# Optimization experiments

Measured on AMD Instinct MI355X. Metric: run time of the kernel, lower is better.

The kernel has to match this reference:

```python
import jax, jax.numpy as jnp
import numpy as np

NV, NSEG, SEGSZ, GRID = 778, 16, 49, 32
SCALE_FACTOR = 0.1


def grid_sample_3d(vol, pts):
    """Trilinear grid_sample, align_corners=True, zeros padding.
    vol: [D,H,W]; pts: [N,3] with (x,y,z) in [-1,1] (x indexes W, z indexes D).
    """
    D, H, W = vol.shape
    fx = (pts[:, 0] + 1.0) * 0.5 * (W - 1)
    fy = (pts[:, 1] + 1.0) * 0.5 * (H - 1)
    fz = (pts[:, 2] + 1.0) * 0.5 * (D - 1)
    x0f, y0f, z0f = jnp.floor(fx), jnp.floor(fy), jnp.floor(fz)
    wx, wy, wz = fx - x0f, fy - y0f, fz - z0f
    x0 = x0f.astype(jnp.int32)
    y0 = y0f.astype(jnp.int32)
    z0 = z0f.astype(jnp.int32)
    out = jnp.zeros(pts.shape[0], vol.dtype)
    for dz in (0, 1):
        zz = z0 + dz
        ww_z = wz if dz else (1.0 - wz)
        for dy in (0, 1):
            yy = y0 + dy
            ww_zy = ww_z * (wy if dy else (1.0 - wy))
            for dx in (0, 1):
                xx = x0 + dx
                w = ww_zy * (wx if dx else (1.0 - wx))
                valid = (xx >= 0) & (xx < W) & (yy >= 0) & (yy < H) & (zz >= 0) & (zz < D)
                v = vol[jnp.clip(zz, 0, D - 1), jnp.clip(yy, 0, H - 1), jnp.clip(xx, 0, W - 1)]
                out = out + jnp.where(valid, v, 0.0) * w
    return out


def _boxes(segv):
    # segv: [B,16,S,3] -> center [B,16,3], scale [B,16]  (no_grad in original)
    mn = segv.min(axis=2)
    mx = segv.max(axis=2)
    center = 0.5 * (mn + mx)                       # mean of (min, max)
    scale = (1.0 + SCALE_FACTOR) * 0.5 * (mx - mn).max(axis=-1)
    return jax.lax.stop_gradient(center), jax.lax.stop_gradient(scale)


def _cross_sample(seg_src, center, scale, phi, seg):
    # seg_src [B,I,S,3]; center [B,J,3]; scale [B,J]; phi [J,B,G,G,G]
    B = seg_src.shape[0]
    coords = (seg_src[:, :, None, :, :] - center[:, None, :, None, :]) / scale[:, None, :, None, None]
    pts = coords.transpose(2, 0, 1, 3, 4).reshape(NSEG, B, NSEG * SEGSZ, 3)  # [J,B,M,3]
    vals = jax.vmap(jax.vmap(grid_sample_3d))(phi, pts)                      # [J,B,M]
    vals = vals.reshape(NSEG, B, NSEG, SEGSZ).transpose(1, 2, 0, 3)          # [B,I,J,S]
    phisum = vals.sum(axis=2)                                                # [B,I,S]
    orisum = (vals * scale[:, None, :, None]).sum(axis=2)                    # [B,I,S]
    flat = seg.reshape(-1)
    out = jnp.zeros((B, NV), jnp.float32).at[:, flat].add(phisum.reshape(B, -1))
    ori = jnp.zeros((B, NV), jnp.float32).at[:, flat].add(orisum.reshape(B, -1))
    return out, ori


def setup_inputs() -> dict:
    key = jax.random.key(0)
    k1, k2, k3, k4 = jax.random.split(key, 4)
    bs = 128
    vertices = jax.random.normal(k1, (bs, 2, NV, 3), dtype=jnp.float32)
    seg = jax.random.randint(k2, (NSEG, SEGSZ), 0, NV).astype(jnp.int32)
    phi_right = jax.random.uniform(k3, (NSEG, bs, GRID, GRID, GRID), dtype=jnp.float32)
    phi_left = jax.random.uniform(k4, (NSEG, bs, GRID, GRID, GRID), dtype=jnp.float32)
    return {"vertices": vertices, "phi_right": phi_right, "phi_left": phi_left, "seg": seg}


def reference(vertices, phi_right, phi_left, seg):
    left_vert = vertices[:, 1]   # [B,778,3]
    right_vert = vertices[:, 0]
    segL = left_vert[:, seg]     # [B,16,S,3]
    segR = right_vert[:, seg]
    cL, sL = _boxes(segL)
    cR, sR = _boxes(segR)
    out_left, _ = _cross_sample(segL, cR, sR, phi_right, seg)
    out_right, _ = _cross_sample(segR, cL, sL, phi_left, seg)
    num_hand = 2
    loss = (out_left / num_hand ** 2 + out_right / num_hand ** 2).sum(axis=1)  # [B]
    return loss
```

## Files before the change

### kernel.cpp

```cpp
#include <hip/hip_runtime.h>

#define NVV   778
#define NSEG  16
#define SEGSZ 49
#define GRIDN 32
#define BATCH 128
#define NPTS  (NSEG * SEGSZ)
#define VOLSZ (GRIDN * GRIDN * GRIDN)
#define NVOL  (2 * BATCH * NSEG)
#define NBLK  256
#define VPB   (NVOL / NBLK)

#define H0_FLOATS (16 * 1024)
#define H1_FLOATS (17 * 1024)
#define H0_CHUNKS (H0_FLOATS / 256)
#define H1_CHUNKS (H1_FLOATS / 256)

typedef __attribute__((address_space(1))) const void* as1_t;
typedef __attribute__((address_space(3))) void* as3_t;

#define STREAM(DST, SRC, NCH) \
    for (int c = wv; c < (NCH); c += 16) { \
        __builtin_amdgcn_global_load_lds( \
            (as1_t)((SRC) + c * 256 + lane * 4), \
            (as3_t)((DST) + c * 256), 16, 0, 0); \
    }

#define PV_LOAD(IT, nx, ny, nz) \
    if ((IT) < VPB && tid < NPTS) { \
        int vid_ = bx + NBLK * (IT); \
        int b_   = (vid_ >> 4) & (BATCH - 1); \
        int src_ = (vid_ >> 11) == 0 ? 1 : 0; \
        const float* v_ = vertices + (((size_t)b_ * 2 + src_) * NVV + pvi) * 3; \
        nx = v_[0]; ny = v_[1]; nz = v_[2]; \
    }

__device__ __forceinline__ float taps_half(
    const float* base, int zrel0, bool z0ok, bool z1ok,
    int x0, int y0, float wx, float wy, float wz)
{
    float s = 0.f;
    #pragma unroll
    for (int dz = 0; dz < 2; ++dz) {
        if (!(dz ? z1ok : z0ok)) continue;
        float wwz = dz ? wz : 1.f - wz;
        const float* slab = base + (zrel0 + dz) * (GRIDN * GRIDN);
        #pragma unroll
        for (int dy = 0; dy < 2; ++dy) {
            int yy = y0 + dy;
            if (yy < 0 || yy >= GRIDN) continue;
            float wzy = wwz * (dy ? wy : 1.f - wy);
            const float* row = slab + yy * GRIDN;
            #pragma unroll
            for (int dx = 0; dx < 2; ++dx) {
                int xx = x0 + dx;
                if (xx < 0 || xx >= GRIDN) continue;
                s += wzy * (dx ? wx : 1.f - wx) * row[xx];
            }
        }
    }
    return s;
}

__global__ __launch_bounds__(1024, 4) void sample_kernel(
    const float* __restrict__ vertices, const int* __restrict__ seg,
    const float* __restrict__ phiR, const float* __restrict__ phiL,
    float* __restrict__ loss)
{
    __shared__ __align__(16) float R0[H0_FLOATS];
    __shared__ __align__(16) float R1[H1_FLOATS];
    __shared__ float4 sbox[VPB];
    __shared__ float wsum[16];

    const int tid  = threadIdx.x;
    const int bx   = blockIdx.x;
    const int k    = bx & (NSEG - 1);
    const int wv   = tid >> 6;
    const int lane = tid & 63;

    auto phiPtr = [&](int it) {
        int vid  = bx + NBLK * it;
        int b    = (vid >> 4) & (BATCH - 1);
        int pass = vid >> 11;
        return (pass == 0 ? phiR : phiL) + ((size_t)k * BATCH + b) * VOLSZ;
    };

    {
        const float* p0 = phiPtr(0);
        STREAM(R0, p0, H0_CHUNKS)
    }

    int pvi = (tid < NPTS) ? seg[tid] : 0;

    {
        int vid  = bx + NBLK * wv;
        int bb   = (vid >> 4) & (BATCH - 1);
        int pass = vid >> 11;
        int boxSide = (pass == 0) ? 0 : 1;
        const float* vbox = vertices + ((size_t)bb * 2 + boxSide) * NVV * 3;
        bool act = lane < SEGSZ;
        int vi = act ? seg[k * SEGSZ + lane] : 0;
        const float* v = vbox + (size_t)vi * 3;
        float x = v[0], y = v[1], z = v[2];
        float mnx = act ? x : 1e30f, mxx = act ? x : -1e30f;
        float mny = act ? y : 1e30f, mxy = act ? y : -1e30f;
        float mnz = act ? z : 1e30f, mxz = act ? z : -1e30f;
        #pragma unroll
        for (int m = 32; m; m >>= 1) {
            mnx = fminf(mnx, __shfl_xor(mnx, m));
            mxx = fmaxf(mxx, __shfl_xor(mxx, m));
            mny = fminf(mny, __shfl_xor(mny, m));
            mxy = fmaxf(mxy, __shfl_xor(mxy, m));
            mnz = fminf(mnz, __shfl_xor(mnz, m));
            mxz = fmaxf(mxz, __shfl_xor(mxz, m));
        }
        if (lane == 0) {
            float ext = fmaxf(fmaxf(mxx - mnx, mxy - mny), mxz - mnz);
            sbox[wv] = make_float4(0.5f * (mnx + mxx), 0.5f * (mny + mxy),
                                   0.5f * (mnz + mxz), 1.0f / (0.55f * ext));
        }
    }

    float pvx = 0.f, pvy = 0.f, pvz = 0.f;
    float nvx = 0.f, nvy = 0.f, nvz = 0.f;
    PV_LOAD(0, pvx, pvy, pvz)

    __syncthreads();

    for (int v = 0; v < VPB; ++v) {
        const float* pv_phi = phiPtr(v);

        STREAM(R1, pv_phi + 15 * 1024, H1_CHUNKS)

        float fx = 0.f, fy = 0.f, fz = -2.f;
        if (tid < NPTS) {
            float4 b4 = sbox[v];
            fx = ((pvx - b4.x) * b4.w + 1.f) * 15.5f;
            fy = ((pvy - b4.y) * b4.w + 1.f) * 15.5f;
            fz = ((pvz - b4.z) * b4.w + 1.f) * 15.5f;
        }
        PV_LOAD(v + 1, nvx, nvy, nvz)

        bool inxy = (fx > -1.f && fx < 32.f && fy > -1.f && fy < 32.f);
        float x0f = floorf(fx), y0f = floorf(fy), z0f = floorf(fz);
        float wx = fx - x0f, wy = fy - y0f, wz = fz - z0f;
        int x0 = (int)x0f, y0 = (int)y0f, z0 = (int)z0f;

        float acc = 0.f;
        if (inxy && fz > -1.f && fz < 15.f)
            acc += taps_half(R0, z0, z0 >= 0, true, x0, y0, wx, wy, wz);

        __syncthreads();

        if (v + 1 < VPB) {
            const float* pn_phi = phiPtr(v + 1);
            STREAM(R0, pn_phi, H0_CHUNKS)
        }
        if (inxy && fz >= 15.f && fz < 32.f)
            acc += taps_half(R1, z0 - 15, true, z0 + 1 < GRIDN, x0, y0, wx, wy, wz);

        #pragma unroll
        for (int off = 32; off; off >>= 1)
            acc += __shfl_down(acc, off);
        if (lane == 0) wsum[wv] = acc;
        __syncthreads();
        if (tid == 0) {
            float tot = 0.f;
            #pragma unroll
            for (int i = 0; i < 16; ++i) tot += wsum[i];
            int vid = bx + NBLK * v;
            atomicAdd(loss + ((vid >> 4) & (BATCH - 1)), tot * 0.25f);
        }
        pvx = nvx; pvy = nvy; pvz = nvz;
    }
}

extern "C" void kernel_launch(void* const* d_in, const int* in_sizes, int n_in,
                              void* d_out, int out_size, void* d_ws, size_t ws_size,
                              hipStream_t stream) {
    const float* vertices = (const float*)d_in[0];
    const float* phiR     = (const float*)d_in[1];
    const float* phiL     = (const float*)d_in[2];
    const int*   seg      = (const int*)d_in[3];
    float* loss = (float*)d_out;

    hipMemsetAsync(d_out, 0, (size_t)out_size * sizeof(float), stream);

    sample_kernel<<<NBLK, 1024, 0, stream>>>(vertices, seg, phiR, phiL, loss);
}
```

Measured before the change: 106.4 us.

## Split volume staging into three overlapping z-slabs with explicit vmcnt waits

Replaces the two-half LDS staging of each 32^3 volume with three 12K-float slabs covering overlapping z-ranges, streamed in rotation so that loading the next volume's slabs overlaps sampling from the current ones. __syncthreads is replaced with inline s_waitcnt vmcnt(N) plus s_barrier, so each wait covers only the required slab instead of draining every outstanding load. The point and box vertex loads are also moved ahead of the first stream. The hand-counted vmcnt values are fragile: if the per-thread load count differs from what is assumed, the kernel could read slabs that have not arrived yet.

Result: no change. 107.5 us (+1.1%).

```diff
diff --git a/kernel.cpp b/kernel.cpp
--- a/kernel.cpp
+++ b/kernel.cpp
@@ -11,20 +11,25 @@
 #define NBLK  256
 #define VPB   (NVOL / NBLK)
 
-#define H0_FLOATS (16 * 1024)
-#define H1_FLOATS (17 * 1024)
-#define H0_CHUNKS (H0_FLOATS / 256)
-#define H1_CHUNKS (H1_FLOATS / 256)
+#define PF      (12 * 1024)
 
 typedef __attribute__((address_space(1))) const void* as1_t;
 typedef __attribute__((address_space(3))) void* as3_t;
 
-#define STREAM(DST, SRC, NCH) \
-    for (int c = wv; c < (NCH); c += 16) { \
+#define STREAM(DST, SRC) \
+    { _Pragma("unroll") \
+      for (int c_ = 0; c_ < 3; ++c_) { \
+        int ch_ = c_ * 16 + wv; \
         __builtin_amdgcn_global_load_lds( \
-            (as1_t)((SRC) + c * 256 + lane * 4), \
-            (as3_t)((DST) + c * 256), 16, 0, 0); \
-    }
+            (as1_t)((SRC) + ch_ * 256 + lane * 4), \
+            (as3_t)((DST) + ch_ * 256), 16, 0, 0); \
+      } }
+
+#define FENCE asm volatile("" ::: "memory")
+
+#define WAITB(N) \
+    { asm volatile("s_waitcnt vmcnt(" #N ") lgkmcnt(0)" ::: "memory"); \
+      __builtin_amdgcn_s_barrier(); }
 
 #define PV_LOAD(IT, nx, ny, nz) \
     if ((IT) < VPB && tid < NPTS) { \
@@ -35,7 +40,7 @@
         nx = v_[0]; ny = v_[1]; nz = v_[2]; \
     }
 
-__device__ __forceinline__ float taps_half(
+__device__ __forceinline__ float taps_piece(
     const float* base, int zrel0, bool z0ok, bool z1ok,
     int x0, int y0, float wx, float wy, float wz)
 {
@@ -67,8 +72,9 @@
     const float* __restrict__ phiR, const float* __restrict__ phiL,
     float* __restrict__ loss)
 {
-    __shared__ __align__(16) float R0[H0_FLOATS];
-    __shared__ __align__(16) float R1[H1_FLOATS];
+    __shared__ __align__(16) float B0[PF];
+    __shared__ __align__(16) float B1[PF];
+    __shared__ __align__(16) float B2[PF];
     __shared__ float4 sbox[VPB];
     __shared__ float wsum[16];
 
@@ -85,26 +91,32 @@
         return (pass == 0 ? phiR : phiL) + ((size_t)k * BATCH + b) * VOLSZ;
     };
 
+    int pvi = (tid < NPTS) ? seg[tid] : 0;
+
+    int vidw  = bx + NBLK * wv;
+    int bbw   = (vidw >> 4) & (BATCH - 1);
+    int boxSide = ((vidw >> 11) == 0) ? 0 : 1;
+    bool bact = lane < SEGSZ;
+    int bvi = bact ? seg[k * SEGSZ + lane] : 0;
+    const float* bv = vertices + (((size_t)bbw * 2 + boxSide) * NVV + bvi) * 3;
+    float bxx = bv[0], bxy = bv[1], bxz = bv[2];
+
+    float pvx = 0.f, pvy = 0.f, pvz = 0.f;
+    float nvx = 0.f, nvy = 0.f, nvz = 0.f;
+    PV_LOAD(0, pvx, pvy, pvz)
+
+    FENCE;
     {
         const float* p0 = phiPtr(0);
-        STREAM(R0, p0, H0_CHUNKS)
-    }
-
-    int pvi = (tid < NPTS) ? seg[tid] : 0;
+        STREAM(B0, p0)
+        STREAM(B1, p0 + 11 * 1024)
+    }
+    FENCE;
 
     {
-        int vid  = bx + NBLK * wv;
-        int bb   = (vid >> 4) & (BATCH - 1);
-        int pass = vid >> 11;
-        int boxSide = (pass == 0) ? 0 : 1;
-        const float* vbox = vertices + ((size_t)bb * 2 + boxSide) * NVV * 3;
-        bool act = lane < SEGSZ;
-        int vi = act ? seg[k * SEGSZ + lane] : 0;
-        const float* v = vbox + (size_t)vi * 3;
-        float x = v[0], y = v[1], z = v[2];
-        float mnx = act ? x : 1e30f, mxx = act ? x : -1e30f;
-        float mny = act ? y : 1e30f, mxy = act ? y : -1e30f;
-        float mnz = act ? z : 1e30f, mxz = act ? z : -1e30f;
+        float mnx = bact ? bxx : 1e30f, mxx = bact ? bxx : -1e30f;
+        float mny = bact ? bxy : 1e30f, mxy = bact ? bxy : -1e30f;
+        float mnz = bact ? bxz : 1e30f, mxz = bact ? bxz : -1e30f;
         #pragma unroll
         for (int m = 32; m; m >>= 1) {
             mnx = fminf(mnx, __shfl_xor(mnx, m));
@@ -121,16 +133,11 @@
         }
     }
 
-    float pvx = 0.f, pvy = 0.f, pvz = 0.f;
-    float nvx = 0.f, nvy = 0.f, nvz = 0.f;
-    PV_LOAD(0, pvx, pvy, pvz)
-
-    __syncthreads();
+    WAITB(3)
 
     for (int v = 0; v < VPB; ++v) {
-        const float* pv_phi = phiPtr(v);
-
-        STREAM(R1, pv_phi + 15 * 1024, H1_CHUNKS)
+        const float* pc_phi = phiPtr(v);
+        const bool more = (v + 1 < VPB);
 
         float fx = 0.f, fy = 0.f, fz = -2.f;
         if (tid < NPTS) {
@@ -139,31 +146,46 @@
             fy = ((pvy - b4.y) * b4.w + 1.f) * 15.5f;
             fz = ((pvz - b4.z) * b4.w + 1.f) * 15.5f;
         }
-        PV_LOAD(v + 1, nvx, nvy, nvz)
-
-        bool inxy = (fx > -1.f && fx < 32.f && fy > -1.f && fy < 32.f);
+        bool active = (fx > -1.f && fx < 32.f && fy > -1.f && fy < 32.f &&
+                       fz > -1.f && fz < 32.f);
         float x0f = floorf(fx), y0f = floorf(fy), z0f = floorf(fz);
         float wx = fx - x0f, wy = fy - y0f, wz = fz - z0f;
         int x0 = (int)x0f, y0 = (int)y0f, z0 = (int)z0f;
-
+        int pc = (z0 <= 10) ? 0 : ((z0 <= 21) ? 1 : 2);
         float acc = 0.f;
-        if (inxy && fz > -1.f && fz < 15.f)
-            acc += taps_half(R0, z0, z0 >= 0, true, x0, y0, wx, wy, wz);
-
-        __syncthreads();
-
-        if (v + 1 < VPB) {
-            const float* pn_phi = phiPtr(v + 1);
-            STREAM(R0, pn_phi, H0_CHUNKS)
-        }
-        if (inxy && fz >= 15.f && fz < 32.f)
-            acc += taps_half(R1, z0 - 15, true, z0 + 1 < GRIDN, x0, y0, wx, wy, wz);
+
+        PV_LOAD(v + 1, nvx, nvy, nvz)
+        FENCE;
+        STREAM(B2, pc_phi + 20 * 1024)
+        FENCE;
+        if (active && pc == 0)
+            acc += taps_piece(B0, z0, z0 >= 0, true, x0, y0, wx, wy, wz);
+        WAITB(3)
+
+        if (more) {
+            const float* pn = phiPtr(v + 1);
+            FENCE;
+            STREAM(B0, pn)
+            FENCE;
+        }
+        if (active && pc == 1)
+            acc += taps_piece(B1, z0 - 11, true, true, x0, y0, wx, wy, wz);
+        if (more) { WAITB(3) } else { WAITB(0) }
+
+        if (more) {
+            const float* pn = phiPtr(v + 1);
+            FENCE;
+            STREAM(B1, pn + 11 * 1024)
+            FENCE;
+        }
+        if (active && pc == 2)
+            acc += taps_piece(B2, z0 - 20, true, z0 < 31, x0, y0, wx, wy, wz);
 
         #pragma unroll
         for (int off = 32; off; off >>= 1)
             acc += __shfl_down(acc, off);
         if (lane == 0) wsum[wv] = acc;
-        __syncthreads();
+        if (more) { WAITB(3) } else { WAITB(0) }
         if (tid == 0) {
             float tot = 0.f;
             #pragma unroll
```

## Split each volume's z-halves across two blocks, drop in-block double buffering

Applied to the files above, without the earlier changes.

Doubles the grid to 512 blocks, with each block handling only one z-half of every volume (17 slabs or 16 slabs) in a single LDS buffer. The previous overlapped two-region streaming pipeline and next-vertex prefetch are removed in favour of load, sync, compute per volume. The aim is to halve LDS per block and raise occupancy so other resident blocks hide load latency. In exchange, box computation and vertex loads are duplicated across the two halves, atomics double, and the in-block load/compute overlap is lost.

Measured after the change: 123.1 us. +15.7%, slower.

```diff
diff --git a/kernel.cpp b/kernel.cpp
--- a/kernel.cpp
+++ b/kernel.cpp
@@ -7,100 +7,49 @@
 #define BATCH 128
 #define NPTS  (NSEG * SEGSZ)
 #define VOLSZ (GRIDN * GRIDN * GRIDN)
-#define NVOL  (2 * BATCH * NSEG)
-#define NBLK  256
-#define VPB   (NVOL / NBLK)
+#define NBLK  512
+#define VPB   16
 
-#define H0_FLOATS (16 * 1024)
-#define H1_FLOATS (17 * 1024)
-#define H0_CHUNKS (H0_FLOATS / 256)
-#define H1_CHUNKS (H1_FLOATS / 256)
+#define HALF_MAX_FLOATS (17 * 1024)
 
 typedef __attribute__((address_space(1))) const void* as1_t;
 typedef __attribute__((address_space(3))) void* as3_t;
 
-#define STREAM(DST, SRC, NCH) \
-    for (int c = wv; c < (NCH); c += 16) { \
-        __builtin_amdgcn_global_load_lds( \
-            (as1_t)((SRC) + c * 256 + lane * 4), \
-            (as3_t)((DST) + c * 256), 16, 0, 0); \
-    }
-
-#define PV_LOAD(IT, nx, ny, nz) \
-    if ((IT) < VPB && tid < NPTS) { \
-        int vid_ = bx + NBLK * (IT); \
-        int b_   = (vid_ >> 4) & (BATCH - 1); \
-        int src_ = (vid_ >> 11) == 0 ? 1 : 0; \
-        const float* v_ = vertices + (((size_t)b_ * 2 + src_) * NVV + pvi) * 3; \
-        nx = v_[0]; ny = v_[1]; nz = v_[2]; \
-    }
-
-__device__ __forceinline__ float taps_half(
-    const float* base, int zrel0, bool z0ok, bool z1ok,
-    int x0, int y0, float wx, float wy, float wz)
-{
-    float s = 0.f;
-    #pragma unroll
-    for (int dz = 0; dz < 2; ++dz) {
-        if (!(dz ? z1ok : z0ok)) continue;
-        float wwz = dz ? wz : 1.f - wz;
-        const float* slab = base + (zrel0 + dz) * (GRIDN * GRIDN);
-        #pragma unroll
-        for (int dy = 0; dy < 2; ++dy) {
-            int yy = y0 + dy;
-            if (yy < 0 || yy >= GRIDN) continue;
-            float wzy = wwz * (dy ? wy : 1.f - wy);
-            const float* row = slab + yy * GRIDN;
-            #pragma unroll
-            for (int dx = 0; dx < 2; ++dx) {
-                int xx = x0 + dx;
-                if (xx < 0 || xx >= GRIDN) continue;
-                s += wzy * (dx ? wx : 1.f - wx) * row[xx];
-            }
-        }
-    }
-    return s;
-}
-
-__global__ __launch_bounds__(1024, 4) void sample_kernel(
+__global__ __launch_bounds__(1024, 8) void sample_kernel(
     const float* __restrict__ vertices, const int* __restrict__ seg,
     const float* __restrict__ phiR, const float* __restrict__ phiL,
     float* __restrict__ loss)
 {
-    __shared__ __align__(16) float R0[H0_FLOATS];
-    __shared__ __align__(16) float R1[H1_FLOATS];
+    __shared__ __align__(16) float piece[HALF_MAX_FLOATS];
     __shared__ float4 sbox[VPB];
     __shared__ float wsum[16];
 
     const int tid  = threadIdx.x;
     const int bx   = blockIdx.x;
-    const int k    = bx & (NSEG - 1);
+    const int half = bx >> 8;
+    const int base = bx & 255;
+    const int k    = base & (NSEG - 1);
     const int wv   = tid >> 6;
     const int lane = tid & 63;
 
+    const int   nch  = half ? 64 : 68;
+    const int   soff = half ? 16 * 1024 : 0;
+
     auto phiPtr = [&](int it) {
-        int vid  = bx + NBLK * it;
+        int vid  = base + 256 * it;
         int b    = (vid >> 4) & (BATCH - 1);
         int pass = vid >> 11;
         return (pass == 0 ? phiR : phiL) + ((size_t)k * BATCH + b) * VOLSZ;
     };
 
+    int pvi = (tid < NPTS) ? seg[tid] : 0;
     {
-        const float* p0 = phiPtr(0);
-        STREAM(R0, p0, H0_CHUNKS)
-    }
-
-    int pvi = (tid < NPTS) ? seg[tid] : 0;
-
-    {
-        int vid  = bx + NBLK * wv;
+        int vid  = base + 256 * wv;
         int bb   = (vid >> 4) & (BATCH - 1);
-        int pass = vid >> 11;
-        int boxSide = (pass == 0) ? 0 : 1;
-        const float* vbox = vertices + ((size_t)bb * 2 + boxSide) * NVV * 3;
+        int boxSide = ((vid >> 11) == 0) ? 0 : 1;
         bool act = lane < SEGSZ;
         int vi = act ? seg[k * SEGSZ + lane] : 0;
-        const float* v = vbox + (size_t)vi * 3;
+        const float* v = vertices + (((size_t)bb * 2 + boxSide) * NVV + vi) * 3;
         float x = v[0], y = v[1], z = v[2];
         float mnx = act ? x : 1e30f, mxx = act ? x : -1e30f;
         float mny = act ? y : 1e30f, mxy = act ? y : -1e30f;
@@ -121,43 +70,62 @@
         }
     }
 
-    float pvx = 0.f, pvy = 0.f, pvz = 0.f;
-    float nvx = 0.f, nvy = 0.f, nvz = 0.f;
-    PV_LOAD(0, pvx, pvy, pvz)
+    for (int it = 0; it < VPB; ++it) {
+        const float* src = phiPtr(it) + soff;
 
-    __syncthreads();
+        for (int c = wv; c < nch; c += 16)
+            __builtin_amdgcn_global_load_lds(
+                (as1_t)(src + c * 256 + lane * 4),
+                (as3_t)(piece + c * 256), 16, 0, 0);
 
-    for (int v = 0; v < VPB; ++v) {
-        const float* pv_phi = phiPtr(v);
-
-        STREAM(R1, pv_phi + 15 * 1024, H1_CHUNKS)
-
-        float fx = 0.f, fy = 0.f, fz = -2.f;
+        float pvx = 0.f, pvy = 0.f, pvz = 0.f;
         if (tid < NPTS) {
-            float4 b4 = sbox[v];
-            fx = ((pvx - b4.x) * b4.w + 1.f) * 15.5f;
-            fy = ((pvy - b4.y) * b4.w + 1.f) * 15.5f;
-            fz = ((pvz - b4.z) * b4.w + 1.f) * 15.5f;
+            int vid  = base + 256 * it;
+            int b    = (vid >> 4) & (BATCH - 1);
+            int srcS = (vid >> 11) == 0 ? 1 : 0;
+            const float* v = vertices + (((size_t)b * 2 + srcS) * NVV + pvi) * 3;
+            pvx = v[0]; pvy = v[1]; pvz = v[2];
         }
-        PV_LOAD(v + 1, nvx, nvy, nvz)
-
-        bool inxy = (fx > -1.f && fx < 32.f && fy > -1.f && fy < 32.f);
-        float x0f = floorf(fx), y0f = floorf(fy), z0f = floorf(fz);
-        float wx = fx - x0f, wy = fy - y0f, wz = fz - z0f;
-        int x0 = (int)x0f, y0 = (int)y0f, z0 = (int)z0f;
-
-        float acc = 0.f;
-        if (inxy && fz > -1.f && fz < 15.f)
-            acc += taps_half(R0, z0, z0 >= 0, true, x0, y0, wx, wy, wz);
 
         __syncthreads();
 
-        if (v + 1 < VPB) {
-            const float* pn_phi = phiPtr(v + 1);
-            STREAM(R0, pn_phi, H0_CHUNKS)
+        float acc = 0.f;
+        if (tid < NPTS) {
+            float4 b4 = sbox[it];
+            float fx = ((pvx - b4.x) * b4.w + 1.f) * 15.5f;
+            float fy = ((pvy - b4.y) * b4.w + 1.f) * 15.5f;
+            float fz = ((pvz - b4.z) * b4.w + 1.f) * 15.5f;
+            bool inxy = (fx > -1.f && fx < 32.f && fy > -1.f && fy < 32.f);
+            bool inz  = half ? (fz >= 16.f && fz < 32.f)
+                             : (fz > -1.f && fz < 16.f);
+            if (inxy && inz) {
+                float x0f = floorf(fx), y0f = floorf(fy), z0f = floorf(fz);
+                float wx = fx - x0f, wy = fy - y0f, wz = fz - z0f;
+                int x0 = (int)x0f, y0 = (int)y0f, z0 = (int)z0f;
+                int zr = z0 - (half ? 16 : 0);
+                bool z0ok = half ? true : (z0 >= 0);
+                bool z1ok = half ? (z0 < 31) : true;
+                #pragma unroll
+                for (int dz = 0; dz < 2; ++dz) {
+                    if (!(dz ? z1ok : z0ok)) continue;
+                    float wwz = dz ? wz : 1.f - wz;
+                    const float* slab = piece + (zr + dz) * (GRIDN * GRIDN);
+                    #pragma unroll
+                    for (int dy = 0; dy < 2; ++dy) {
+                        int yy = y0 + dy;
+                        if (yy < 0 || yy >= GRIDN) continue;
+                        float wzy = wwz * (dy ? wy : 1.f - wy);
+                        const float* row = slab + yy * GRIDN;
+                        #pragma unroll
+                        for (int dx = 0; dx < 2; ++dx) {
+                            int xx = x0 + dx;
+                            if (xx < 0 || xx >= GRIDN) continue;
+                            acc += wzy * (dx ? wx : 1.f - wx) * row[xx];
+                        }
+                    }
+                }
+            }
         }
-        if (inxy && fz >= 15.f && fz < 32.f)
-            acc += taps_half(R1, z0 - 15, true, z0 + 1 < GRIDN, x0, y0, wx, wy, wz);
 
         #pragma unroll
         for (int off = 32; off; off >>= 1)
@@ -168,10 +136,9 @@
             float tot = 0.f;
             #pragma unroll
             for (int i = 0; i < 16; ++i) tot += wsum[i];
-            int vid = bx + NBLK * v;
+            int vid = base + 256 * it;
             atomicAdd(loss + ((vid >> 4) & (BATCH - 1)), tot * 0.25f);
         }
-        pvx = nvx; pvy = nvy; pvz = nvz;
     }
 }
 
```

## Split volume into equal 16-slab halves, per-wave atomics, restructure loads

Applied to the files above, without the earlier changes.

The volume is now split into two equal 16-slab halves instead of 16 and 17 slabs with an overlap slab. The straddling z=15/16 case is handled by sampling one tap plane from each buffer, so the LDS streaming loops become fixed four-iteration unrolled loops. The block-level reduction through shared memory and thread 0 is replaced by a per-wave atomicAdd to global memory. The prefetch of the next vertices is moved after the barrier. This trims redundant LDS traffic and one reduction step, at the cost of sixteen times more global atomics per volume.

Measured after the change: 323.3 us. +203.9%, slower.

```diff
diff --git a/kernel.cpp b/kernel.cpp
--- a/kernel.cpp
+++ b/kernel.cpp
@@ -7,56 +7,38 @@
 #define BATCH 128
 #define NPTS  (NSEG * SEGSZ)
 #define VOLSZ (GRIDN * GRIDN * GRIDN)
-#define NVOL  (2 * BATCH * NSEG)
 #define NBLK  256
-#define VPB   (NVOL / NBLK)
+#define VPB   16
 
-#define H0_FLOATS (16 * 1024)
-#define H1_FLOATS (17 * 1024)
-#define H0_CHUNKS (H0_FLOATS / 256)
-#define H1_CHUNKS (H1_FLOATS / 256)
+#define HF (16 * 1024)
 
 typedef __attribute__((address_space(1))) const void* as1_t;
 typedef __attribute__((address_space(3))) void* as3_t;
 
-#define STREAM(DST, SRC, NCH) \
-    for (int c = wv; c < (NCH); c += 16) { \
+#define STREAM(DST, SRC) \
+    { _Pragma("unroll") \
+      for (int c_ = 0; c_ < 4; ++c_) { \
+        int ch_ = c_ * 16 + wv; \
         __builtin_amdgcn_global_load_lds( \
-            (as1_t)((SRC) + c * 256 + lane * 4), \
-            (as3_t)((DST) + c * 256), 16, 0, 0); \
-    }
+            (as1_t)((SRC) + ch_ * 256 + lane * 4), \
+            (as3_t)((DST) + ch_ * 256), 16, 0, 0); \
+      } }
 
-#define PV_LOAD(IT, nx, ny, nz) \
-    if ((IT) < VPB && tid < NPTS) { \
-        int vid_ = bx + NBLK * (IT); \
-        int b_   = (vid_ >> 4) & (BATCH - 1); \
-        int src_ = (vid_ >> 11) == 0 ? 1 : 0; \
-        const float* v_ = vertices + (((size_t)b_ * 2 + src_) * NVV + pvi) * 3; \
-        nx = v_[0]; ny = v_[1]; nz = v_[2]; \
-    }
-
-__device__ __forceinline__ float taps_half(
-    const float* base, int zrel0, bool z0ok, bool z1ok,
-    int x0, int y0, float wx, float wy, float wz)
+__device__ __forceinline__ float tapxy(const float* slab, int x0, int y0,
+                                       float wx, float wy)
 {
     float s = 0.f;
     #pragma unroll
-    for (int dz = 0; dz < 2; ++dz) {
-        if (!(dz ? z1ok : z0ok)) continue;
-        float wwz = dz ? wz : 1.f - wz;
-        const float* slab = base + (zrel0 + dz) * (GRIDN * GRIDN);
+    for (int dy = 0; dy < 2; ++dy) {
+        int yy = y0 + dy;
+        if (yy < 0 || yy >= GRIDN) continue;
+        float wyv = dy ? wy : 1.f - wy;
+        const float* row = slab + yy * GRIDN;
         #pragma unroll
-        for (int dy = 0; dy < 2; ++dy) {
-            int yy = y0 + dy;
-            if (yy < 0 || yy >= GRIDN) continue;
-            float wzy = wwz * (dy ? wy : 1.f - wy);
-            const float* row = slab + yy * GRIDN;
-            #pragma unroll
-            for (int dx = 0; dx < 2; ++dx) {
-                int xx = x0 + dx;
-                if (xx < 0 || xx >= GRIDN) continue;
-                s += wzy * (dx ? wx : 1.f - wx) * row[xx];
-            }
+        for (int dx = 0; dx < 2; ++dx) {
+            int xx = x0 + dx;
+            if (xx < 0 || xx >= GRIDN) continue;
+            s += wyv * (dx ? wx : 1.f - wx) * row[xx];
         }
     }
     return s;
@@ -67,10 +49,9 @@
     const float* __restrict__ phiR, const float* __restrict__ phiL,
     float* __restrict__ loss)
 {
-    __shared__ __align__(16) float R0[H0_FLOATS];
-    __shared__ __align__(16) float R1[H1_FLOATS];
+    __shared__ __align__(16) float R0[HF];
+    __shared__ __align__(16) float R1[HF];
     __shared__ float4 sbox[VPB];
-    __shared__ float wsum[16];
 
     const int tid  = threadIdx.x;
     const int bx   = blockIdx.x;
@@ -85,26 +66,30 @@
         return (pass == 0 ? phiR : phiL) + ((size_t)k * BATCH + b) * VOLSZ;
     };
 
-    {
-        const float* p0 = phiPtr(0);
-        STREAM(R0, p0, H0_CHUNKS)
+    int pvi = (tid < NPTS) ? seg[tid] : 0;
+
+    int vidw    = bx + NBLK * wv;
+    int bbw     = (vidw >> 4) & (BATCH - 1);
+    int boxSide = ((vidw >> 11) == 0) ? 0 : 1;
+    bool bact   = lane < SEGSZ;
+    int bvi     = bact ? seg[k * SEGSZ + lane] : 0;
+    const float* bvp = vertices + (((size_t)bbw * 2 + boxSide) * NVV + bvi) * 3;
+    float bxx = bvp[0], bxy = bvp[1], bxz = bvp[2];
+
+    float pvx = 0.f, pvy = 0.f, pvz = 0.f;
+    if (tid < NPTS) {
+        int srcS = 1;
+        int b0   = (bx >> 4) & (BATCH - 1);
+        const float* v = vertices + (((size_t)b0 * 2 + srcS) * NVV + pvi) * 3;
+        pvx = v[0]; pvy = v[1]; pvz = v[2];
     }
 
-    int pvi = (tid < NPTS) ? seg[tid] : 0;
+    STREAM(R0, phiPtr(0))
 
     {
-        int vid  = bx + NBLK * wv;
-        int bb   = (vid >> 4) & (BATCH - 1);
-        int pass = vid >> 11;
-        int boxSide = (pass == 0) ? 0 : 1;
-        const float* vbox = vertices + ((size_t)bb * 2 + boxSide) * NVV * 3;
-        bool act = lane < SEGSZ;
-        int vi = act ? seg[k * SEGSZ + lane] : 0;
-        const float* v = vbox + (size_t)vi * 3;
-        float x = v[0], y = v[1], z = v[2];
-        float mnx = act ? x : 1e30f, mxx = act ? x : -1e30f;
-        float mny = act ? y : 1e30f, mxy = act ? y : -1e30f;
-        float mnz = act ? z : 1e30f, mxz = act ? z : -1e30f;
+        float mnx = bact ? bxx : 1e30f, mxx = bact ? bxx : -1e30f;
+        float mny = bact ? bxy : 1e30f, mxy = bact ? bxy : -1e30f;
+        float mnz = bact ? bxz : 1e30f, mxz = bact ? bxz : -1e30f;
         #pragma unroll
         for (int m = 32; m; m >>= 1) {
             mnx = fminf(mnx, __shfl_xor(mnx, m));
@@ -121,16 +106,14 @@
         }
     }
 
-    float pvx = 0.f, pvy = 0.f, pvz = 0.f;
-    float nvx = 0.f, nvy = 0.f, nvz = 0.f;
-    PV_LOAD(0, pvx, pvy, pvz)
-
     __syncthreads();
 
+    float nvx = 0.f, nvy = 0.f, nvz = 0.f;
+
     for (int v = 0; v < VPB; ++v) {
-        const float* pv_phi = phiPtr(v);
+        const bool more = (v + 1 < VPB);
 
-        STREAM(R1, pv_phi + 15 * 1024, H1_CHUNKS)
+        STREAM(R1, phiPtr(v) + HF)
 
         float fx = 0.f, fy = 0.f, fz = -2.f;
         if (tid < NPTS) {
@@ -139,38 +122,47 @@
             fy = ((pvy - b4.y) * b4.w + 1.f) * 15.5f;
             fz = ((pvz - b4.z) * b4.w + 1.f) * 15.5f;
         }
-        PV_LOAD(v + 1, nvx, nvy, nvz)
-
-        bool inxy = (fx > -1.f && fx < 32.f && fy > -1.f && fy < 32.f);
+        bool active = (fx > -1.f && fx < 32.f && fy > -1.f && fy < 32.f &&
+                       fz > -1.f && fz < 32.f);
         float x0f = floorf(fx), y0f = floorf(fy), z0f = floorf(fz);
         float wx = fx - x0f, wy = fy - y0f, wz = fz - z0f;
         int x0 = (int)x0f, y0 = (int)y0f, z0 = (int)z0f;
 
         float acc = 0.f;
-        if (inxy && fz > -1.f && fz < 15.f)
-            acc += taps_half(R0, z0, z0 >= 0, true, x0, y0, wx, wy, wz);
+        if (active && z0 <= 15) {
+            if (z0 >= 0)
+                acc += (1.f - wz) * tapxy(R0 + z0 * 1024, x0, y0, wx, wy);
+            if (z0 <= 14)
+                acc += wz * tapxy(R0 + (z0 + 1) * 1024, x0, y0, wx, wy);
+        }
 
         __syncthreads();
 
-        if (v + 1 < VPB) {
-            const float* pn_phi = phiPtr(v + 1);
-            STREAM(R0, pn_phi, H0_CHUNKS)
+        if (more && tid < NPTS) {
+            int vid  = bx + NBLK * (v + 1);
+            int b_   = (vid >> 4) & (BATCH - 1);
+            int srcS = (vid >> 11) == 0 ? 1 : 0;
+            const float* vp = vertices + (((size_t)b_ * 2 + srcS) * NVV + pvi) * 3;
+            nvx = vp[0]; nvy = vp[1]; nvz = vp[2];
         }
-        if (inxy && fz >= 15.f && fz < 32.f)
-            acc += taps_half(R1, z0 - 15, true, z0 + 1 < GRIDN, x0, y0, wx, wy, wz);
+        if (more) { STREAM(R0, phiPtr(v + 1)) }
+
+        if (active && z0 >= 15) {
+            if (z0 >= 16)
+                acc += (1.f - wz) * tapxy(R1 + (z0 - 16) * 1024, x0, y0, wx, wy);
+            if (z0 <= 30)
+                acc += wz * tapxy(R1 + (z0 - 15) * 1024, x0, y0, wx, wy);
+        }
 
         #pragma unroll
         for (int off = 32; off; off >>= 1)
             acc += __shfl_down(acc, off);
-        if (lane == 0) wsum[wv] = acc;
+        if (lane == 0) {
+            int vid = bx + NBLK * v;
+            atomicAdd(loss + ((vid >> 4) & (BATCH - 1)), acc * 0.25f);
+        }
+
         __syncthreads();
-        if (tid == 0) {
-            float tot = 0.f;
-            #pragma unroll
-            for (int i = 0; i < 16; ++i) tot += wsum[i];
-            int vid = bx + NBLK * v;
-            atomicAdd(loss + ((vid >> 4) & (BATCH - 1)), tot * 0.25f);
-        }
         pvx = nvx; pvy = nvy; pvz = nvz;
     }
 }
```
